# Kernel tuning notes

Measured on AMD Instinct MI355X. Metric: run time of the kernel, lower is better.

The kernel has to match this reference:

```python
import jax, jax.numpy as jnp
import numpy as np

B, T, D_IN, H1, H2 = 1024, 512, 128, 100, 100


def setup_inputs() -> dict:
    key = jax.random.key(0)
    ks = jax.random.split(key, 9)
    s1 = 1.0 / np.sqrt(H1)  # PyTorch LSTMCell init scale
    s2 = 1.0 / np.sqrt(H2)
    return {
        "x": jax.random.normal(ks[0], (B, T, D_IN), dtype=jnp.float32),
        "W_ih1": jax.random.normal(ks[1], (4 * H1, D_IN), dtype=jnp.float32) * s1,
        "W_hh1": jax.random.normal(ks[2], (4 * H1, H1), dtype=jnp.float32) * s1,
        "b_ih1": jax.random.normal(ks[3], (4 * H1,), dtype=jnp.float32) * s1,
        "b_hh1": jax.random.normal(ks[4], (4 * H1,), dtype=jnp.float32) * s1,
        "W_ih2": jax.random.normal(ks[5], (4 * H2, H1), dtype=jnp.float32) * s2,
        "W_hh2": jax.random.normal(ks[6], (4 * H2, H2), dtype=jnp.float32) * s2,
        "b_ih2": jax.random.normal(ks[7], (4 * H2,), dtype=jnp.float32) * s2,
        "b_hh2": jax.random.normal(ks[8], (4 * H2,), dtype=jnp.float32) * s2,
    }


def _lstm_cell(xt, h, c, W_ih, W_hh, b_ih, b_hh, H):
    # PyTorch LSTMCell: gates = x@W_ih^T + b_ih + h@W_hh^T + b_hh, chunked i,f,g,o
    gates = xt @ W_ih.T + h @ W_hh.T + (b_ih + b_hh)
    i = jax.nn.sigmoid(gates[:, 0 * H:1 * H])
    f = jax.nn.sigmoid(gates[:, 1 * H:2 * H])
    g = jnp.tanh(gates[:, 2 * H:3 * H])
    o = jax.nn.sigmoid(gates[:, 3 * H:4 * H])
    c_new = f * c + i * g
    h_new = o * jnp.tanh(c_new)
    return h_new, c_new


def reference(x, W_ih1, W_hh1, b_ih1, b_hh1, W_ih2, W_hh2, b_ih2, b_hh2):
    Bsz = x.shape[0]
    h1 = jnp.zeros((Bsz, H1), x.dtype)
    c1 = jnp.zeros((Bsz, H1), x.dtype)
    h2 = jnp.zeros((Bsz, H2), x.dtype)
    c2 = jnp.zeros((Bsz, H2), x.dtype)

    def step(carry, xt):
        h1, c1, h2, c2 = carry
        h1, c1 = _lstm_cell(xt, h1, c1, W_ih1, W_hh1, b_ih1, b_hh1, H1)
        # dropout(0.25) between layers: identity in eval mode (deterministic baseline)
        h2, c2 = _lstm_cell(h1, h2, c2, W_ih2, W_hh2, b_ih2, b_hh2, H2)
        return (h1, c1, h2, c2), h2

    xs = jnp.swapaxes(x, 0, 1)  # [T, B, D]
    _, ys = jax.lax.scan(step, (h1, c1, h2, c2), xs)
    return jnp.swapaxes(ys, 0, 1)  # [B, T, H2]
```

## Files before the change

### kernel.cpp

```cpp
#include <hip/hip_runtime.h>

#define B_TOT 1024
#define T_LEN 512
#define D_INP 128
#define H 100
#define HP 112
#define HX 128
#define NP 448
#define NT_TILES 28
#define FRAG_ELEMS 57344

#define LOG2E  1.4426950408889634f
#define LOG2E2 2.8853900817779268f

typedef _Float16 half8 __attribute__((ext_vector_type(8)));
typedef _Float16 half4 __attribute__((ext_vector_type(4)));
typedef float f32x4 __attribute__((ext_vector_type(4)));

#if __has_builtin(__builtin_amdgcn_exp2f)
__device__ __forceinline__ float EXP2(float x) { return __builtin_amdgcn_exp2f(x); }
#else
__device__ __forceinline__ float EXP2(float x) { return __expf(x * 0.6931471805599453f); }
#endif
#if __has_builtin(__builtin_amdgcn_rcpf)
__device__ __forceinline__ float RCP(float x) { return __builtin_amdgcn_rcpf(x); }
#else
__device__ __forceinline__ float RCP(float x) { return 1.0f / x; }
#endif

__device__ __forceinline__ float sig2(float zp) {
    return RCP(1.0f + EXP2(-zp));
}
__device__ __forceinline__ float tanh2(float zp) {
    return 1.0f - 2.0f * RCP(EXP2(zp) + 1.0f);
}
__device__ __forceinline__ float tanhc(float c) {
    return 1.0f - 2.0f * RCP(EXP2(c * LOG2E2) + 1.0f);
}

__device__ __forceinline__ float fast_sigmoid(float z) {
    return RCP(1.0f + EXP2(-z * LOG2E));
}
__device__ __forceinline__ float fast_tanh(float z) {
    return 1.0f - 2.0f * RCP(EXP2(z * LOG2E2) + 1.0f);
}

__device__ __forceinline__ unsigned pack2(float x, float y) {
    _Float16 a = (_Float16)x, b = (_Float16)y;
    unsigned short ua = __builtin_bit_cast(unsigned short, a);
    unsigned short ub = __builtin_bit_cast(unsigned short, b);
    return (unsigned)ua | ((unsigned)ub << 16);
}
__device__ __forceinline__ unsigned swz(int row, int colbyte) {
    return ((unsigned)row * 256u + (unsigned)colbyte) ^ (unsigned)((row & 7) << 4);
}
__device__ __forceinline__ void step_barrier() {
    asm volatile("s_waitcnt lgkmcnt(0)\n\ts_barrier" ::: "memory");
}

__global__ void init_states(float* s, int n) {
    int i = blockIdx.x * 256 + threadIdx.x;
    if (i < n) s[i] = 0.f;
}

__global__ void prep_frags(const float* __restrict__ Wih1, const float* __restrict__ Wih2,
                           const float* __restrict__ Whh1, const float* __restrict__ Whh2,
                           const float* __restrict__ bih1, const float* __restrict__ bhh1,
                           const float* __restrict__ bih2, const float* __restrict__ bhh2,
                           _Float16* __restrict__ frags, float* __restrict__ biases)
{
    int i = blockIdx.x * 256 + threadIdx.x;
    if (i < 4 * FRAG_ELEMS) {
        int sec = i / FRAG_ELEMS, j = i % FRAG_ELEMS;
        int e = j & 7, lane = (j >> 3) & 63, kt = (j >> 9) & 3, nt = j >> 11;
        int l = lane & 15, jb = nt >> 2, g = nt & 3;
        int hcol = jb * 16 + l;
        int k = kt * 32 + (lane >> 4) * 8 + e;
        const float* W = (sec == 0) ? Wih1 : (sec == 1) ? Wih2 : (sec == 2) ? Whh1 : Whh2;
        int Kreal = (sec == 0) ? 128 : 100;
        float v = 0.f;
        if (hcol < 100 && k < Kreal)
            v = W[(g * 100 + hcol) * Kreal + k] * ((g == 2) ? LOG2E2 : LOG2E);
        frags[i] = (_Float16)v;
        return;
    }
    i -= 4 * FRAG_ELEMS;
    if (i < 2 * NP) {
        int layer = i / NP, cp = i % NP;
        int jb = cp >> 6, g = (cp >> 4) & 3, l = cp & 15;
        int hcol = jb * 16 + l;
        float v = 0.f;
        if (hcol < 100) {
            int G = g * 100 + hcol;
            v = (layer ? (bih2[G] + bhh2[G]) : (bih1[G] + bhh1[G]))
              * ((g == 2) ? LOG2E2 : LOG2E);
        }
        biases[i] = v;
    }
}

template<int CT>
__global__ __launch_bounds__(512, 2) void superstep(
    const float* __restrict__ x,
    const _Float16* __restrict__ wfrag1, const float* __restrict__ bias1,
    _Float16* __restrict__ X1w, const _Float16* __restrict__ X1r,
    const _Float16* __restrict__ whhf1, _Float16* __restrict__ h1w,
    _Float16* __restrict__ hst1, float* __restrict__ cst1,
    const _Float16* __restrict__ h1r,
    const _Float16* __restrict__ wihf2, const _Float16* __restrict__ whhf2,
    const float* __restrict__ bias2p,
    _Float16* __restrict__ hst2, float* __restrict__ cst2,
    float* __restrict__ out,
    int t0g, int r1on, int t0r2)
{
    __shared__ __align__(16) unsigned char smem[65536 + 2048];
    const int tid = threadIdx.x;
    const int blk = blockIdx.x;

    if (blk < 64) {
        if (!r1on) return;
        unsigned char* hr0 = smem;
        unsigned char* hr1 = smem + 4096;
        const int w = tid >> 6, lane = tid & 63;
        const bool active = w < 7;
        const int jb = w, l = lane & 15, rg = lane >> 4;
        const int bg = blk, b0 = bg * 16;
        const int col = jb * 16 + l;

        unsigned rdo[4], wro[4];
        #pragma unroll
        for (int kt = 0; kt < 4; ++kt) rdo[kt] = swz(l, (kt * 32 + rg * 8) * 2);
        #pragma unroll
        for (int r = 0; r < 4; ++r) wro[r] = swz(rg * 4 + r, col * 2);

        half8 bf[4][4];
        float cst[4];
        half4 xP[4];
        const _Float16* x_p[4];
        _Float16* hs_p[4];
        if (active) {
            #pragma unroll
            for (int g = 0; g < 4; ++g)
                #pragma unroll
                for (int kt = 0; kt < 4; ++kt)
                    bf[g][kt] = *reinterpret_cast<const half8*>(
                        whhf1 + (((long)(jb * 4 + g) * 4 + kt) * 64 + lane) * 8);
            const _Float16* xb = X1r + (size_t)bg * CT * 16 * NP + jb * 64 + l * 4;
            #pragma unroll
            for (int r = 0; r < 4; ++r) {
                cst[r] = cst1[(size_t)(b0 + rg * 4 + r) * HP + col];
                x_p[r] = xb + (size_t)(rg * 4 + r) * NP;
                hs_p[r] = h1w + (size_t)bg * CT * 16 * HX + (size_t)(rg * 4 + r) * HX + col;
                xP[r] = *reinterpret_cast<const half4*>(x_p[r]);
                x_p[r] += (size_t)16 * NP;
            }
        }
        if (tid < 64) {
            int buf = tid >> 5, r2i = (tid & 31) >> 1, c8 = 112 + (tid & 1) * 8;
            *reinterpret_cast<uint4*>((buf ? hr1 : hr0) + swz(r2i, c8 * 2)) = make_uint4(0u, 0u, 0u, 0u);
        }
        if (tid >= 64 && tid < 288) {
            int i = tid - 64, row = i / 14, c8 = (i % 14) * 8;
            *reinterpret_cast<uint4*>(hr1 + swz(row, c8 * 2)) =
                *reinterpret_cast<const uint4*>(hst1 + (size_t)(b0 + row) * HP + c8);
        }
        __syncthreads();

        auto STEP1 = [&](int it, const unsigned char* rb, unsigned char* wb)
            __attribute__((always_inline)) {
            half8 af[4];
            #pragma unroll
            for (int kt = 0; kt < 4; ++kt)
                af[kt] = *reinterpret_cast<const half8*>(rb + rdo[kt]);
            f32x4 acc[4];
            #pragma unroll
            for (int g = 0; g < 4; ++g)
                #pragma unroll
                for (int r = 0; r < 4; ++r) acc[g][r] = (float)xP[r][g];
            if (it + 1 < CT) {
                #pragma unroll
                for (int r = 0; r < 4; ++r) {
                    xP[r] = *reinterpret_cast<const half4*>(x_p[r]);
                    x_p[r] += (size_t)16 * NP;
                }
            }
            #pragma unroll
            for (int kt = 0; kt < 4; ++kt)
                #pragma unroll
                for (int g = 0; g < 4; ++g)
                    acc[g] = __builtin_amdgcn_mfma_f32_16x16x32_f16(af[kt], bf[g][kt], acc[g], 0, 0, 0);
            #pragma unroll
            for (int r = 0; r < 4; ++r) {
                float ig = sig2(acc[0][r]);
                float fg = sig2(acc[1][r]);
                float gg = tanh2(acc[2][r]);
                float og = sig2(acc[3][r]);
                float c = fg * cst[r] + ig * gg;
                cst[r] = c;
                float h = og * tanhc(c);
                _Float16 hf = (_Float16)h;
                *reinterpret_cast<_Float16*>(wb + wro[r]) = hf;
                *hs_p[r] = hf;
                hs_p[r] += (size_t)16 * HX;
            }
        };

        for (int it = 0; it < CT; it += 2) {
            if (active) STEP1(it, hr1, hr0);
            step_barrier();
            if (active) STEP1(it + 1, hr0, hr1);
            step_barrier();
        }

        if (active) {
            #pragma unroll
            for (int r = 0; r < 4; ++r)
                cst1[(size_t)(b0 + rg * 4 + r) * HP + col] = cst[r];
        }
        if (tid < 224) {
            int row = tid / 14, c8 = (tid % 14) * 8;
            const unsigned char* sbuf = ((CT - 1) & 1) ? hr1 : hr0;
            *reinterpret_cast<uint4*>(hst1 + (size_t)(b0 + row) * HP + c8) =
                *reinterpret_cast<const uint4*>(sbuf + swz(row, c8 * 2));
        }
        return;
    }

    if (blk < 128) {
        if (t0r2 < 0) return;
        unsigned char* hr0 = smem;
        unsigned char* hr1 = smem + 4096;
        const int w = tid >> 6, lane = tid & 63;
        const bool active = w < 7;
        const int jb = w, l = lane & 15, rg = lane >> 4;
        const int bg = blk - 64, b0 = bg * 16;
        const int col = jb * 16 + l;

        unsigned rdo[4], wro[4];
        #pragma unroll
        for (int kt = 0; kt < 4; ++kt) rdo[kt] = swz(l, (kt * 32 + rg * 8) * 2);
        #pragma unroll
        for (int r = 0; r < 4; ++r) wro[r] = swz(rg * 4 + r, col * 2);

        half8 bi[4][4], bh[4][4];
        float b2v[4];
        float cst[4];
        half8 hP[4];
        const _Float16* hb_p = nullptr;
        float* out_p[4];
        if (active) {
            #pragma unroll
            for (int g = 0; g < 4; ++g)
                #pragma unroll
                for (int kt = 0; kt < 4; ++kt) {
                    long o = (((long)(jb * 4 + g) * 4 + kt) * 64 + lane) * 8;
                    bi[g][kt] = *reinterpret_cast<const half8*>(wihf2 + o);
                    bh[g][kt] = *reinterpret_cast<const half8*>(whhf2 + o);
                }
            #pragma unroll
            for (int g = 0; g < 4; ++g) b2v[g] = bias2p[jb * 64 + g * 16 + l];
            hb_p = h1r + (size_t)bg * CT * 16 * HX + (size_t)l * HX + rg * 8;
            #pragma unroll
            for (int r = 0; r < 4; ++r) {
                cst[r] = cst2[(size_t)(b0 + rg * 4 + r) * HP + col];
                out_p[r] = out + ((size_t)(b0 + rg * 4 + r) * T_LEN + t0r2) * H + col;
            }
            #pragma unroll
            for (int kt = 0; kt < 4; ++kt)
                hP[kt] = *reinterpret_cast<const half8*>(hb_p + kt * 32);
        }
        if (tid < 64) {
            int buf = tid >> 5, r2i = (tid & 31) >> 1, c8 = 112 + (tid & 1) * 8;
            *reinterpret_cast<uint4*>((buf ? hr1 : hr0) + swz(r2i, c8 * 2)) = make_uint4(0u, 0u, 0u, 0u);
        }
        if (tid >= 64 && tid < 288) {
            int i = tid - 64, row = i / 14, c8 = (i % 14) * 8;
            *reinterpret_cast<uint4*>(hr1 + swz(row, c8 * 2)) =
                *reinterpret_cast<const uint4*>(hst2 + (size_t)(b0 + row) * HP + c8);
        }
        __syncthreads();

        auto STEP2 = [&](int it, const unsigned char* rb, unsigned char* wb)
            __attribute__((always_inline)) {
            half8 af2[4];
            #pragma unroll
            for (int kt = 0; kt < 4; ++kt)
                af2[kt] = *reinterpret_cast<const half8*>(rb + rdo[kt]);
            f32x4 acc[4];
            #pragma unroll
            for (int g = 0; g < 4; ++g)
                acc[g] = (f32x4){b2v[g], b2v[g], b2v[g], b2v[g]};
            #pragma unroll
            for (int kt = 0; kt < 4; ++kt)
                #pragma unroll
                for (int g = 0; g < 4; ++g)
                    acc[g] = __builtin_amdgcn_mfma_f32_16x16x32_f16(hP[kt], bi[g][kt], acc[g], 0, 0, 0);
            if (it + 1 < CT) {
                hb_p += (size_t)16 * HX;
                #pragma unroll
                for (int kt = 0; kt < 4; ++kt)
                    hP[kt] = *reinterpret_cast<const half8*>(hb_p + kt * 32);
            }
            #pragma unroll
            for (int kt = 0; kt < 4; ++kt)
                #pragma unroll
                for (int g = 0; g < 4; ++g)
                    acc[g] = __builtin_amdgcn_mfma_f32_16x16x32_f16(af2[kt], bh[g][kt], acc[g], 0, 0, 0);
            #pragma unroll
            for (int r = 0; r < 4; ++r) {
                float ig = sig2(acc[0][r]);
                float fg = sig2(acc[1][r]);
                float gg = tanh2(acc[2][r]);
                float og = sig2(acc[3][r]);
                float c = fg * cst[r] + ig * gg;
                cst[r] = c;
                float h = og * tanhc(c);
                *reinterpret_cast<_Float16*>(wb + wro[r]) = (_Float16)h;
                if (col < H) *out_p[r] = h;
                out_p[r] += H;
            }
        };

        for (int it = 0; it < CT; it += 2) {
            if (active) STEP2(it, hr1, hr0);
            step_barrier();
            if (active) STEP2(it + 1, hr0, hr1);
            step_barrier();
        }

        if (active) {
            #pragma unroll
            for (int r = 0; r < 4; ++r)
                cst2[(size_t)(b0 + rg * 4 + r) * HP + col] = cst[r];
        }
        if (tid < 224) {
            int row = tid / 14, c8 = (tid % 14) * 8;
            const unsigned char* sbuf = ((CT - 1) & 1) ? hr1 : hr0;
            *reinterpret_cast<uint4*>(hst2 + (size_t)(b0 + row) * HP + c8) =
                *reinterpret_cast<const uint4*>(sbuf + swz(row, c8 * 2));
        }
        return;
    }

    if (t0g < 0) return;
    {
        constexpr int LOG2CT = (CT == 128) ? 7 : (CT == 64) ? 6 : 5;
        unsigned char* sA = smem;
        float* sBias = reinterpret_cast<float*>(smem + 65536);
        const long row0 = (long)(blk - 128) * 256;

        {
            const int r = tid >> 1, kh = (tid & 1) * 64;
            long rr = row0 + r;
            long b = rr >> LOG2CT; int tc = (int)(rr & (CT - 1));
            const float* src = x + (b * T_LEN + t0g + tc) * D_INP;
            #pragma unroll
            for (int i = 0; i < 16; ++i) {
                int k = kh + i * 4;
                float4 v = *reinterpret_cast<const float4*>(src + k);
                unsigned off = ((unsigned)r * 256u + (unsigned)k * 2u) ^ (unsigned)((r & 7) << 4);
                *reinterpret_cast<uint2*>(sA + off) = make_uint2(pack2(v.x, v.y), pack2(v.z, v.w));
            }
        }
        for (int i = tid; i < NP; i += 512) sBias[i] = bias1[i];
        __syncthreads();

        const int wv = tid >> 6, lane = tid & 63;
        const int lrow = lane & 15, lk = (lane >> 4) * 8;

        half8 aF[2][4];
        #pragma unroll
        for (int s = 0; s < 2; ++s)
            #pragma unroll
            for (int kt = 0; kt < 4; ++kt) {
                int rowL = wv * 32 + s * 16 + lrow;
                unsigned off = ((unsigned)rowL * 256u + (unsigned)(kt * 32 + lk) * 2u)
                             ^ (unsigned)((rowL & 7) << 4);
                aF[s][kt] = *reinterpret_cast<const half8*>(sA + off);
            }

        size_t obase[2][4];
        #pragma unroll
        for (int s = 0; s < 2; ++s)
            #pragma unroll
            for (int r = 0; r < 4; ++r) {
                long rgl = row0 + wv * 32 + s * 16 + (lane >> 4) * 4 + r;
                long b = rgl >> LOG2CT; int tc = (int)(rgl & (CT - 1));
                obase[s][r] = (((size_t)(b >> 4) * CT + tc) * 16 + (b & 15)) * NP;
            }

        for (int nt = 0; nt < NT_TILES; ++nt) {
            half8 bF[4];
            const _Float16* bp = wfrag1 + ((long)(nt * 4) * 64 + lane) * 8;
            #pragma unroll
            for (int kt = 0; kt < 4; ++kt)
                bF[kt] = *reinterpret_cast<const half8*>(bp + (long)kt * 512);

            f32x4 acc0 = {0.f, 0.f, 0.f, 0.f}, acc1 = {0.f, 0.f, 0.f, 0.f};
            #pragma unroll
            for (int kt = 0; kt < 4; ++kt) {
                acc0 = __builtin_amdgcn_mfma_f32_16x16x32_f16(aF[0][kt], bF[kt], acc0, 0, 0, 0);
                acc1 = __builtin_amdgcn_mfma_f32_16x16x32_f16(aF[1][kt], bF[kt], acc1, 0, 0, 0);
            }
            const int col = nt * 16 + lrow;
            const int pcol = (col & ~63) | ((col & 15) << 2) | ((col >> 4) & 3);
            const float bv = sBias[col];
            #pragma unroll
            for (int r = 0; r < 4; ++r) {
                X1w[obase[0][r] + pcol] = (_Float16)(acc0[r] + bv);
                X1w[obase[1][r] + pcol] = (_Float16)(acc1[r] + bv);
            }
        }
    }
}

__global__ __launch_bounds__(256) void lstm2_persistent(
    const float* __restrict__ x,
    const float* __restrict__ W_ih1, const float* __restrict__ W_hh1,
    const float* __restrict__ b_ih1, const float* __restrict__ b_hh1,
    const float* __restrict__ W_ih2, const float* __restrict__ W_hh2,
    const float* __restrict__ b_ih2, const float* __restrict__ b_hh2,
    float* __restrict__ out)
{
    __shared__ float s_x[4][D_INP];
    __shared__ float s_h1[4][H], s_c1[4][H], s_h2[4][H], s_c2[4][H];
    __shared__ float s_g[4][400];
    __shared__ float s_b1[400], s_b2[400];
    const int tid = threadIdx.x;
    const int row0 = blockIdx.x * 4;
    for (int i = tid; i < 400; i += 256) { s_b1[i] = b_ih1[i] + b_hh1[i]; s_b2[i] = b_ih2[i] + b_hh2[i]; }
    for (int i = tid; i < 4 * H; i += 256) { int r = i / H, jj = i % H;
        s_h1[r][jj] = 0.f; s_c1[r][jj] = 0.f; s_h2[r][jj] = 0.f; s_c2[r][jj] = 0.f; }
    __syncthreads();
    for (int t = 0; t < T_LEN; ++t) {
        for (int i = tid; i < 4 * D_INP; i += 256) { int r = i >> 7, d = i & 127;
            s_x[r][d] = x[((size_t)(row0 + r) * T_LEN + t) * D_INP + d]; }
        __syncthreads();
        for (int g = tid; g < 400; g += 256) {
            float a0, a1, a2, a3; a0 = a1 = a2 = a3 = s_b1[g];
            const float4* wi = reinterpret_cast<const float4*>(W_ih1 + (size_t)g * D_INP);
            for (int d4 = 0; d4 < D_INP / 4; ++d4) {
                float4 wv = wi[d4];
                float4 v0 = *reinterpret_cast<const float4*>(&s_x[0][d4 * 4]);
                float4 v1 = *reinterpret_cast<const float4*>(&s_x[1][d4 * 4]);
                float4 v2 = *reinterpret_cast<const float4*>(&s_x[2][d4 * 4]);
                float4 v3 = *reinterpret_cast<const float4*>(&s_x[3][d4 * 4]);
                a0 += wv.x*v0.x + wv.y*v0.y + wv.z*v0.z + wv.w*v0.w;
                a1 += wv.x*v1.x + wv.y*v1.y + wv.z*v1.z + wv.w*v1.w;
                a2 += wv.x*v2.x + wv.y*v2.y + wv.z*v2.z + wv.w*v2.w;
                a3 += wv.x*v3.x + wv.y*v3.y + wv.z*v3.z + wv.w*v3.w;
            }
            const float4* wh = reinterpret_cast<const float4*>(W_hh1 + (size_t)g * H);
            for (int k4 = 0; k4 < H / 4; ++k4) {
                float4 wv = wh[k4];
                float4 v0 = *reinterpret_cast<const float4*>(&s_h1[0][k4 * 4]);
                float4 v1 = *reinterpret_cast<const float4*>(&s_h1[1][k4 * 4]);
                float4 v2 = *reinterpret_cast<const float4*>(&s_h1[2][k4 * 4]);
                float4 v3 = *reinterpret_cast<const float4*>(&s_h1[3][k4 * 4]);
                a0 += wv.x*v0.x + wv.y*v0.y + wv.z*v0.z + wv.w*v0.w;
                a1 += wv.x*v1.x + wv.y*v1.y + wv.z*v1.z + wv.w*v1.w;
                a2 += wv.x*v2.x + wv.y*v2.y + wv.z*v2.z + wv.w*v2.w;
                a3 += wv.x*v3.x + wv.y*v3.y + wv.z*v3.z + wv.w*v3.w;
            }
            s_g[0][g] = a0; s_g[1][g] = a1; s_g[2][g] = a2; s_g[3][g] = a3;
        }
        __syncthreads();
        for (int idx = tid; idx < 4 * H; idx += 256) {
            int r = idx / H, jj = idx % H;
            float ig = fast_sigmoid(s_g[r][jj]);
            float fg = fast_sigmoid(s_g[r][H + jj]);
            float gg = fast_tanh(s_g[r][2 * H + jj]);
            float og = fast_sigmoid(s_g[r][3 * H + jj]);
            float cc = fg * s_c1[r][jj] + ig * gg;
            s_c1[r][jj] = cc; s_h1[r][jj] = og * fast_tanh(cc);
        }
        __syncthreads();
        for (int g = tid; g < 400; g += 256) {
            float a0, a1, a2, a3; a0 = a1 = a2 = a3 = s_b2[g];
            const float4* wi = reinterpret_cast<const float4*>(W_ih2 + (size_t)g * H);
            const float4* wh = reinterpret_cast<const float4*>(W_hh2 + (size_t)g * H);
            for (int k4 = 0; k4 < H / 4; ++k4) {
                float4 wv = wi[k4];
                float4 v0 = *reinterpret_cast<const float4*>(&s_h1[0][k4 * 4]);
                float4 v1 = *reinterpret_cast<const float4*>(&s_h1[1][k4 * 4]);
                float4 v2 = *reinterpret_cast<const float4*>(&s_h1[2][k4 * 4]);
                float4 v3 = *reinterpret_cast<const float4*>(&s_h1[3][k4 * 4]);
                a0 += wv.x*v0.x + wv.y*v0.y + wv.z*v0.z + wv.w*v0.w;
                a1 += wv.x*v1.x + wv.y*v1.y + wv.z*v1.z + wv.w*v1.w;
                a2 += wv.x*v2.x + wv.y*v2.y + wv.z*v2.z + wv.w*v2.w;
                a3 += wv.x*v3.x + wv.y*v3.y + wv.z*v3.z + wv.w*v3.w;
            }
            for (int k4 = 0; k4 < H / 4; ++k4) {
                float4 wv = wh[k4];
                float4 v0 = *reinterpret_cast<const float4*>(&s_h2[0][k4 * 4]);
                float4 v1 = *reinterpret_cast<const float4*>(&s_h2[1][k4 * 4]);
                float4 v2 = *reinterpret_cast<const float4*>(&s_h2[2][k4 * 4]);
                float4 v3 = *reinterpret_cast<const float4*>(&s_h2[3][k4 * 4]);
                a0 += wv.x*v0.x + wv.y*v0.y + wv.z*v0.z + wv.w*v0.w;
                a1 += wv.x*v1.x + wv.y*v1.y + wv.z*v1.z + wv.w*v1.w;
                a2 += wv.x*v2.x + wv.y*v2.y + wv.z*v2.z + wv.w*v2.w;
                a3 += wv.x*v3.x + wv.y*v3.y + wv.z*v3.z + wv.w*v3.w;
            }
            s_g[0][g] = a0; s_g[1][g] = a1; s_g[2][g] = a2; s_g[3][g] = a3;
        }
        __syncthreads();
        for (int idx = tid; idx < 4 * H; idx += 256) {
            int r = idx / H, jj = idx % H;
            float ig = fast_sigmoid(s_g[r][jj]);
            float fg = fast_sigmoid(s_g[r][H + jj]);
            float gg = fast_tanh(s_g[r][2 * H + jj]);
            float og = fast_sigmoid(s_g[r][3 * H + jj]);
            float cc = fg * s_c2[r][jj] + ig * gg;
            s_c2[r][jj] = cc;
            float hn = og * fast_tanh(cc);
            s_h2[r][jj] = hn;
            out[((size_t)(row0 + r) * T_LEN + t) * H + jj] = hn;
        }
        __syncthreads();
    }
}

template<int CT>
static void run_pipeline(const float* x, float* out,
                         _Float16* X1a, _Float16* X1b, _Float16* h1a, _Float16* h1b,
                         float* cst1, float* cst2, _Float16* hst1, _Float16* hst2,
                         const _Float16* wfrag1, const _Float16* wihf2,
                         const _Float16* whhf1, const _Float16* whhf2,
                         const float* bias1, const float* bias2,
                         hipStream_t stream)
{
    const int nCh = T_LEN / CT;
    const unsigned grid = 128u + (unsigned)((size_t)B_TOT * CT / 256);
    for (int k = 0; k <= nCh + 1; ++k) {
        int t0g  = (k < nCh) ? k * CT : -1;
        int r1on = (k >= 1 && k <= nCh) ? 1 : 0;
        int t0r2 = (k >= 2) ? (k - 2) * CT : -1;
        _Float16* X1w = (k & 1) ? X1b : X1a;
        const _Float16* X1r = (k & 1) ? X1a : X1b;
        _Float16* h1w = (k & 1) ? h1a : h1b;
        const _Float16* h1r = (k & 1) ? h1b : h1a;
        superstep<CT><<<grid, 512, 0, stream>>>(
            x, wfrag1, bias1, X1w, X1r,
            whhf1, h1w, hst1, cst1,
            h1r, wihf2, whhf2, bias2, hst2, cst2, out,
            t0g, r1on, t0r2);
    }
}

extern "C" void kernel_launch(void* const* d_in, const int* in_sizes, int n_in,
                              void* d_out, int out_size, void* d_ws, size_t ws_size,
                              hipStream_t stream) {
    const float* x     = (const float*)d_in[0];
    const float* W_ih1 = (const float*)d_in[1];
    const float* W_hh1 = (const float*)d_in[2];
    const float* b_ih1 = (const float*)d_in[3];
    const float* b_hh1 = (const float*)d_in[4];
    const float* W_ih2 = (const float*)d_in[5];
    const float* W_hh2 = (const float*)d_in[6];
    const float* b_ih2 = (const float*)d_in[7];
    const float* b_hh2 = (const float*)d_in[8];
    float* out = (float*)d_out;

    auto need = [](int CT) -> size_t {
        return 2ull * B_TOT * CT * NP * 2
             + 2ull * B_TOT * CT * HX * 2
             + 2ull * B_TOT * HP * 4
             + 2ull * B_TOT * HP * 2
             + 4ull * FRAG_ELEMS * 2
             + 2ull * NP * 4
             + 256;
    };

    int CT = 0;
    if (ws_size >= need(64)) CT = 64;
    else if (ws_size >= need(32)) CT = 32;

    if (CT == 0) {
        lstm2_persistent<<<B_TOT / 4, 256, 0, stream>>>(
            x, W_ih1, W_hh1, b_ih1, b_hh1, W_ih2, W_hh2, b_ih2, b_hh2, out);
        return;
    }

    char* p = (char*)d_ws;
    _Float16* X1a = (_Float16*)p;     p += (size_t)B_TOT * CT * NP * 2;
    _Float16* X1b = (_Float16*)p;     p += (size_t)B_TOT * CT * NP * 2;
    _Float16* h1a = (_Float16*)p;     p += (size_t)B_TOT * CT * HX * 2;
    _Float16* h1b = (_Float16*)p;     p += (size_t)B_TOT * CT * HX * 2;
    float* cst1 = (float*)p;          p += (size_t)B_TOT * HP * 4;
    float* cst2 = (float*)p;          p += (size_t)B_TOT * HP * 4;
    _Float16* hst1 = (_Float16*)p;    p += (size_t)B_TOT * HP * 2;
    _Float16* hst2 = (_Float16*)p;    p += (size_t)B_TOT * HP * 2;
    _Float16* frags = (_Float16*)p;   p += 4ull * FRAG_ELEMS * 2;
    float* biases = (float*)p;        p += 2ull * NP * 4;

    const _Float16* wfrag1 = frags;
    const _Float16* wihf2  = frags + FRAG_ELEMS;
    const _Float16* whhf1  = frags + 2ull * FRAG_ELEMS;
    const _Float16* whhf2  = frags + 3ull * FRAG_ELEMS;
    const float* bias1 = biases;
    const float* bias2 = biases + NP;

    int nzero = 3 * B_TOT * HP;
    init_states<<<(nzero + 255) / 256, 256, 0, stream>>>(cst1, nzero);

    int nprep = 4 * FRAG_ELEMS + 2 * NP;
    prep_frags<<<(nprep + 255) / 256, 256, 0, stream>>>(
        W_ih1, W_ih2, W_hh1, W_hh2, b_ih1, b_hh1, b_ih2, b_hh2, frags, biases);

    if (CT == 64)
        run_pipeline<64>(x, out, X1a, X1b, h1a, h1b, cst1, cst2, hst1, hst2,
                         wfrag1, wihf2, whhf1, whhf2, bias1, bias2, stream);
    else
        run_pipeline<32>(x, out, X1a, X1b, h1a, h1b, cst1, cst2, hst1, hst2,
                         wfrag1, wihf2, whhf1, whhf2, bias1, bias2, stream);
}
```

Baseline: 775.8 us.

## Hoist layer-2 input projection into a separate parallel GEMM pipeline stage

Layer 2's input projection (h1 @ W_ih2) is taken out of the sequential recurrence and run as a batched MFMA GEMM stage by extra blocks. It writes a precomputed X2 buffer that the layer-2 recurrent blocks then read, the same way layer 1 reads X1. This shortens the serial per-step critical path and frees registers, so launch bounds go from 2 to 4 waves per EU. The cost is one more pipeline stage (one extra launch), a larger grid, and extra workspace plus memory traffic for the X2 buffers.

```diff
diff --git a/kernel.cpp b/kernel.cpp
--- a/kernel.cpp
+++ b/kernel.cpp
@@ -28,22 +28,11 @@
 __device__ __forceinline__ float RCP(float x) { return 1.0f / x; }
 #endif
 
-__device__ __forceinline__ float sig2(float zp) {
-    return RCP(1.0f + EXP2(-zp));
-}
-__device__ __forceinline__ float tanh2(float zp) {
-    return 1.0f - 2.0f * RCP(EXP2(zp) + 1.0f);
-}
-__device__ __forceinline__ float tanhc(float c) {
-    return 1.0f - 2.0f * RCP(EXP2(c * LOG2E2) + 1.0f);
-}
-
-__device__ __forceinline__ float fast_sigmoid(float z) {
-    return RCP(1.0f + EXP2(-z * LOG2E));
-}
-__device__ __forceinline__ float fast_tanh(float z) {
-    return 1.0f - 2.0f * RCP(EXP2(z * LOG2E2) + 1.0f);
-}
+__device__ __forceinline__ float sig2(float zp)  { return RCP(1.0f + EXP2(-zp)); }
+__device__ __forceinline__ float tanh2(float zp) { return 1.0f - 2.0f * RCP(EXP2(zp) + 1.0f); }
+__device__ __forceinline__ float tanhc(float c)  { return 1.0f - 2.0f * RCP(EXP2(c * LOG2E2) + 1.0f); }
+__device__ __forceinline__ float fast_sigmoid(float z) { return RCP(1.0f + EXP2(-z * LOG2E)); }
+__device__ __forceinline__ float fast_tanh(float z)    { return 1.0f - 2.0f * RCP(EXP2(z * LOG2E2) + 1.0f); }
 
 __device__ __forceinline__ unsigned pack2(float x, float y) {
     _Float16 a = (_Float16)x, b = (_Float16)y;
@@ -100,19 +89,23 @@
 }
 
 template<int CT>
-__global__ __launch_bounds__(512, 2) void superstep(
+__global__ __launch_bounds__(512, 4) void superstep(
     const float* __restrict__ x,
     const _Float16* __restrict__ wfrag1, const float* __restrict__ bias1,
     _Float16* __restrict__ X1w, const _Float16* __restrict__ X1r,
     const _Float16* __restrict__ whhf1, _Float16* __restrict__ h1w,
     _Float16* __restrict__ hst1, float* __restrict__ cst1,
-    const _Float16* __restrict__ h1r,
-    const _Float16* __restrict__ wihf2, const _Float16* __restrict__ whhf2,
-    const float* __restrict__ bias2p,
+    const _Float16* __restrict__ h1g,
+    const _Float16* __restrict__ wihf2, const float* __restrict__ bias2p,
+    _Float16* __restrict__ X2w,
+    const _Float16* __restrict__ X2r,
+    const _Float16* __restrict__ whhf2,
     _Float16* __restrict__ hst2, float* __restrict__ cst2,
     float* __restrict__ out,
-    int t0g, int r1on, int t0r2)
+    int t0g, int r1on, int g2on, int t0r2)
 {
+    constexpr int Ng = (B_TOT / 256) * CT;
+    constexpr int LOG2CT = (CT == 128) ? 7 : (CT == 64) ? 6 : 5;
     __shared__ __align__(16) unsigned char smem[65536 + 2048];
     const int tid = threadIdx.x;
     const int blk = blockIdx.x;
@@ -136,8 +129,8 @@
         half8 bf[4][4];
         float cst[4];
         half4 xP[4];
-        const _Float16* x_p[4];
-        _Float16* hs_p[4];
+        const _Float16* x_p = nullptr;
+        _Float16* hs_p = nullptr;
         if (active) {
             #pragma unroll
             for (int g = 0; g < 4; ++g)
@@ -145,15 +138,14 @@
                 for (int kt = 0; kt < 4; ++kt)
                     bf[g][kt] = *reinterpret_cast<const half8*>(
                         whhf1 + (((long)(jb * 4 + g) * 4 + kt) * 64 + lane) * 8);
-            const _Float16* xb = X1r + (size_t)bg * CT * 16 * NP + jb * 64 + l * 4;
+            x_p = X1r + (size_t)bg * CT * 16 * NP + (size_t)(rg * 4) * NP + jb * 64 + l * 4;
+            hs_p = h1w + (size_t)bg * CT * 16 * HX + (size_t)(rg * 4) * HX + col;
             #pragma unroll
             for (int r = 0; r < 4; ++r) {
                 cst[r] = cst1[(size_t)(b0 + rg * 4 + r) * HP + col];
-                x_p[r] = xb + (size_t)(rg * 4 + r) * NP;
-                hs_p[r] = h1w + (size_t)bg * CT * 16 * HX + (size_t)(rg * 4 + r) * HX + col;
-                xP[r] = *reinterpret_cast<const half4*>(x_p[r]);
-                x_p[r] += (size_t)16 * NP;
-            }
+                xP[r] = *reinterpret_cast<const half4*>(x_p + (size_t)r * NP);
+            }
+            x_p += (size_t)16 * NP;
         }
         if (tid < 64) {
             int buf = tid >> 5, r2i = (tid & 31) >> 1, c8 = 112 + (tid & 1) * 8;
@@ -179,10 +171,9 @@
                 for (int r = 0; r < 4; ++r) acc[g][r] = (float)xP[r][g];
             if (it + 1 < CT) {
                 #pragma unroll
-                for (int r = 0; r < 4; ++r) {
-                    xP[r] = *reinterpret_cast<const half4*>(x_p[r]);
-                    x_p[r] += (size_t)16 * NP;
-                }
+                for (int r = 0; r < 4; ++r)
+                    xP[r] = *reinterpret_cast<const half4*>(x_p + (size_t)r * NP);
+                x_p += (size_t)16 * NP;
             }
             #pragma unroll
             for (int kt = 0; kt < 4; ++kt)
@@ -200,9 +191,9 @@
                 float h = og * tanhc(c);
                 _Float16 hf = (_Float16)h;
                 *reinterpret_cast<_Float16*>(wb + wro[r]) = hf;
-                *hs_p[r] = hf;
-                hs_p[r] += (size_t)16 * HX;
-            }
+                *(hs_p + (size_t)r * HX) = hf;
+            }
+            hs_p += (size_t)16 * HX;
         };
 
         for (int it = 0; it < CT; it += 2) {
@@ -242,32 +233,26 @@
         #pragma unroll
         for (int r = 0; r < 4; ++r) wro[r] = swz(rg * 4 + r, col * 2);
 
-        half8 bi[4][4], bh[4][4];
-        float b2v[4];
+        half8 bh[4][4];
         float cst[4];
-        half8 hP[4];
-        const _Float16* hb_p = nullptr;
-        float* out_p[4];
+        half4 xP[4];
+        const _Float16* x2_p = nullptr;
+        float* out_p = nullptr;
         if (active) {
             #pragma unroll
             for (int g = 0; g < 4; ++g)
                 #pragma unroll
-                for (int kt = 0; kt < 4; ++kt) {
-                    long o = (((long)(jb * 4 + g) * 4 + kt) * 64 + lane) * 8;
-                    bi[g][kt] = *reinterpret_cast<const half8*>(wihf2 + o);
-                    bh[g][kt] = *reinterpret_cast<const half8*>(whhf2 + o);
-                }
-            #pragma unroll
-            for (int g = 0; g < 4; ++g) b2v[g] = bias2p[jb * 64 + g * 16 + l];
-            hb_p = h1r + (size_t)bg * CT * 16 * HX + (size_t)l * HX + rg * 8;
+                for (int kt = 0; kt < 4; ++kt)
+                    bh[g][kt] = *reinterpret_cast<const half8*>(
+                        whhf2 + (((long)(jb * 4 + g) * 4 + kt) * 64 + lane) * 8);
+            x2_p = X2r + (size_t)bg * CT * 16 * NP + (size_t)(rg * 4) * NP + jb * 64 + l * 4;
+            out_p = out + ((size_t)(b0 + rg * 4) * T_LEN + t0r2) * H + col;
             #pragma unroll
             for (int r = 0; r < 4; ++r) {
                 cst[r] = cst2[(size_t)(b0 + rg * 4 + r) * HP + col];
-                out_p[r] = out + ((size_t)(b0 + rg * 4 + r) * T_LEN + t0r2) * H + col;
-            }
-            #pragma unroll
-            for (int kt = 0; kt < 4; ++kt)
-                hP[kt] = *reinterpret_cast<const half8*>(hb_p + kt * 32);
+                xP[r] = *reinterpret_cast<const half4*>(x2_p + (size_t)r * NP);
+            }
+            x2_p += (size_t)16 * NP;
         }
         if (tid < 64) {
             int buf = tid >> 5, r2i = (tid & 31) >> 1, c8 = 112 + (tid & 1) * 8;
@@ -289,17 +274,13 @@
             f32x4 acc[4];
             #pragma unroll
             for (int g = 0; g < 4; ++g)
-                acc[g] = (f32x4){b2v[g], b2v[g], b2v[g], b2v[g]};
-            #pragma unroll
-            for (int kt = 0; kt < 4; ++kt)
-                #pragma unroll
-                for (int g = 0; g < 4; ++g)
-                    acc[g] = __builtin_amdgcn_mfma_f32_16x16x32_f16(hP[kt], bi[g][kt], acc[g], 0, 0, 0);
+                #pragma unroll
+                for (int r = 0; r < 4; ++r) acc[g][r] = (float)xP[r][g];
             if (it + 1 < CT) {
-                hb_p += (size_t)16 * HX;
-                #pragma unroll
-                for (int kt = 0; kt < 4; ++kt)
-                    hP[kt] = *reinterpret_cast<const half8*>(hb_p + kt * 32);
+                #pragma unroll
+                for (int r = 0; r < 4; ++r)
+                    xP[r] = *reinterpret_cast<const half4*>(x2_p + (size_t)r * NP);
+                x2_p += (size_t)16 * NP;
             }
             #pragma unroll
             for (int kt = 0; kt < 4; ++kt)
@@ -316,9 +297,9 @@
                 cst[r] = c;
                 float h = og * tanhc(c);
                 *reinterpret_cast<_Float16*>(wb + wro[r]) = (_Float16)h;
-                if (col < H) *out_p[r] = h;
-                out_p[r] += H;
-            }
+                if (col < H) *(out_p + (size_t)r * T_LEN * H) = h;
+            }
+            out_p += H;
         };
 
         for (int it = 0; it < CT; it += 2) {
@@ -342,15 +323,15 @@
         return;
     }
 
-    if (t0g < 0) return;
-    {
-        constexpr int LOG2CT = (CT == 128) ? 7 : (CT == 64) ? 6 : 5;
+    if (blk < 128 + Ng) {
+        if (t0g < 0) return;
         unsigned char* sA = smem;
         float* sBias = reinterpret_cast<float*>(smem + 65536);
         const long row0 = (long)(blk - 128) * 256;
+        const int tid_ = tid;
 
         {
-            const int r = tid >> 1, kh = (tid & 1) * 64;
+            const int r = tid_ >> 1, kh = (tid_ & 1) * 64;
             long rr = row0 + r;
             long b = rr >> LOG2CT; int tc = (int)(rr & (CT - 1));
             const float* src = x + (b * T_LEN + t0g + tc) * D_INP;
@@ -362,10 +343,10 @@
                 *reinterpret_cast<uint2*>(sA + off) = make_uint2(pack2(v.x, v.y), pack2(v.z, v.w));
             }
         }
-        for (int i = tid; i < NP; i += 512) sBias[i] = bias1[i];
-        __syncthreads();
-
-        const int wv = tid >> 6, lane = tid & 63;
+        for (int i = tid_; i < NP; i += 512) sBias[i] = bias1[i];
+        __syncthreads();
+
+        const int wv = tid_ >> 6, lane = tid_ & 63;
         const int lrow = lane & 15, lk = (lane >> 4) * 8;
 
         half8 aF[2][4];
@@ -379,14 +360,14 @@
                 aF[s][kt] = *reinterpret_cast<const half8*>(sA + off);
             }
 
-        size_t obase[2][4];
+        unsigned ob[2][4];
         #pragma unroll
         for (int s = 0; s < 2; ++s)
             #pragma unroll
             for (int r = 0; r < 4; ++r) {
                 long rgl = row0 + wv * 32 + s * 16 + (lane >> 4) * 4 + r;
                 long b = rgl >> LOG2CT; int tc = (int)(rgl & (CT - 1));
-                obase[s][r] = (((size_t)(b >> 4) * CT + tc) * 16 + (b & 15)) * NP;
+                ob[s][r] = (unsigned)((((b >> 4) * CT + tc) * 16 + (b & 15)) * NP);
             }
 
         for (int nt = 0; nt < NT_TILES; ++nt) {
@@ -407,8 +388,60 @@
             const float bv = sBias[col];
             #pragma unroll
             for (int r = 0; r < 4; ++r) {
-                X1w[obase[0][r] + pcol] = (_Float16)(acc0[r] + bv);
-                X1w[obase[1][r] + pcol] = (_Float16)(acc1[r] + bv);
+                X1w[ob[0][r] + pcol] = (_Float16)(acc0[r] + bv);
+                X1w[ob[1][r] + pcol] = (_Float16)(acc1[r] + bv);
+            }
+        }
+        return;
+    }
+
+    {
+        if (!g2on) return;
+        const long row0 = (long)(blk - 128 - Ng) * 256;
+        const int wv = tid >> 6, lane = tid & 63;
+        const int lrow = lane & 15, lk = (lane >> 4) * 8;
+
+        half8 aG[2][4];
+        #pragma unroll
+        for (int s = 0; s < 2; ++s) {
+            long rgl = row0 + wv * 32 + s * 16 + lrow;
+            long b = rgl >> LOG2CT; int tc = (int)(rgl & (CT - 1));
+            const _Float16* ap = h1g + (((size_t)(b >> 4) * CT + tc) * 16 + (b & 15)) * HX + lk;
+            #pragma unroll
+            for (int kt = 0; kt < 4; ++kt)
+                aG[s][kt] = *reinterpret_cast<const half8*>(ap + kt * 32);
+        }
+
+        unsigned ob[2][4];
+        #pragma unroll
+        for (int s = 0; s < 2; ++s)
+            #pragma unroll
+            for (int r = 0; r < 4; ++r) {
+                long rgl = row0 + wv * 32 + s * 16 + (lane >> 4) * 4 + r;
+                long b = rgl >> LOG2CT; int tc = (int)(rgl & (CT - 1));
+                ob[s][r] = (unsigned)((((b >> 4) * CT + tc) * 16 + (b & 15)) * NP);
+            }
+
+        for (int nt = 0; nt < NT_TILES; ++nt) {
+            half8 bF[4];
+            const _Float16* bp = wihf2 + ((long)(nt * 4) * 64 + lane) * 8;
+            #pragma unroll
+            for (int kt = 0; kt < 4; ++kt)
+                bF[kt] = *reinterpret_cast<const half8*>(bp + (long)kt * 512);
+
+            f32x4 acc0 = {0.f, 0.f, 0.f, 0.f}, acc1 = {0.f, 0.f, 0.f, 0.f};
+            #pragma unroll
+            for (int kt = 0; kt < 4; ++kt) {
+                acc0 = __builtin_amdgcn_mfma_f32_16x16x32_f16(aG[0][kt], bF[kt], acc0, 0, 0, 0);
+                acc1 = __builtin_amdgcn_mfma_f32_16x16x32_f16(aG[1][kt], bF[kt], acc1, 0, 0, 0);
+            }
+            const int col = nt * 16 + lrow;
+            const int pcol = (col & ~63) | ((col & 15) << 2) | ((col >> 4) & 3);
+            const float bv = bias2p[col];
+            #pragma unroll
+            for (int r = 0; r < 4; ++r) {
+                X2w[ob[0][r] + pcol] = (_Float16)(acc0[r] + bv);
+                X2w[ob[1][r] + pcol] = (_Float16)(acc1[r] + bv);
             }
         }
     }
@@ -523,6 +556,7 @@
 template<int CT>
 static void run_pipeline(const float* x, float* out,
                          _Float16* X1a, _Float16* X1b, _Float16* h1a, _Float16* h1b,
+                         _Float16* X2a, _Float16* X2b,
                          float* cst1, float* cst2, _Float16* hst1, _Float16* hst2,
                          const _Float16* wfrag1, const _Float16* wihf2,
                          const _Float16* whhf1, const _Float16* whhf2,
@@ -530,20 +564,25 @@
                          hipStream_t stream)
 {
     const int nCh = T_LEN / CT;
-    const unsigned grid = 128u + (unsigned)((size_t)B_TOT * CT / 256);
-    for (int k = 0; k <= nCh + 1; ++k) {
+    const unsigned Ng = (unsigned)((B_TOT / 256) * CT);
+    const unsigned grid = 128u + 2u * Ng;
+    for (int k = 0; k <= nCh + 2; ++k) {
         int t0g  = (k < nCh) ? k * CT : -1;
         int r1on = (k >= 1 && k <= nCh) ? 1 : 0;
-        int t0r2 = (k >= 2) ? (k - 2) * CT : -1;
+        int g2on = (k >= 2 && k <= nCh + 1) ? 1 : 0;
+        int t0r2 = (k >= 3 && k <= nCh + 2) ? (k - 3) * CT : -1;
         _Float16* X1w = (k & 1) ? X1b : X1a;
         const _Float16* X1r = (k & 1) ? X1a : X1b;
         _Float16* h1w = (k & 1) ? h1a : h1b;
-        const _Float16* h1r = (k & 1) ? h1b : h1a;
+        const _Float16* h1g = (k & 1) ? h1b : h1a;
+        _Float16* X2w = (k & 1) ? X2b : X2a;
+        const _Float16* X2r = (k & 1) ? X2a : X2b;
         superstep<CT><<<grid, 512, 0, stream>>>(
             x, wfrag1, bias1, X1w, X1r,
             whhf1, h1w, hst1, cst1,
-            h1r, wihf2, whhf2, bias2, hst2, cst2, out,
-            t0g, r1on, t0r2);
+            h1g, wihf2, bias2, X2w, X2r,
+            whhf2, hst2, cst2, out,
+            t0g, r1on, g2on, t0r2);
     }
 }
 
@@ -563,6 +602,7 @@
 
     auto need = [](int CT) -> size_t {
         return 2ull * B_TOT * CT * NP * 2
+             + 2ull * B_TOT * CT * NP * 2
              + 2ull * B_TOT * CT * HX * 2
              + 2ull * B_TOT * HP * 4
              + 2ull * B_TOT * HP * 2
@@ -584,6 +624,8 @@
     char* p = (char*)d_ws;
     _Float16* X1a = (_Float16*)p;     p += (size_t)B_TOT * CT * NP * 2;
     _Float16* X1b = (_Float16*)p;     p += (size_t)B_TOT * CT * NP * 2;
+    _Float16* X2a = (_Float16*)p;     p += (size_t)B_TOT * CT * NP * 2;
+    _Float16* X2b = (_Float16*)p;     p += (size_t)B_TOT * CT * NP * 2;
     _Float16* h1a = (_Float16*)p;     p += (size_t)B_TOT * CT * HX * 2;
     _Float16* h1b = (_Float16*)p;     p += (size_t)B_TOT * CT * HX * 2;
     float* cst1 = (float*)p;          p += (size_t)B_TOT * HP * 4;
@@ -608,9 +650,9 @@
         W_ih1, W_ih2, W_hh1, W_hh2, b_ih1, b_hh1, b_ih2, b_hh2, frags, biases);
 
     if (CT == 64)
-        run_pipeline<64>(x, out, X1a, X1b, h1a, h1b, cst1, cst2, hst1, hst2,
+        run_pipeline<64>(x, out, X1a, X1b, h1a, h1b, X2a, X2b, cst1, cst2, hst1, hst2,
                          wfrag1, wihf2, whhf1, whhf2, bias1, bias2, stream);
     else
-        run_pipeline<32>(x, out, X1a, X1b, h1a, h1b, cst1, cst2, hst1, hst2,
+        run_pipeline<32>(x, out, X1a, X1b, h1a, h1b, X2a, X2b, cst1, cst2, hst1, hst2,
                          wfrag1, wihf2, whhf1, whhf2, bias1, bias2, stream);
 }
```

After: 1.313 ms. 69.2% more time.
